# Kernel optimization log

Hardware: AMD Instinct MI355X
Metric: run time of the kernel (lower is better)

Reference implementation:

```python
import jax, jax.numpy as jnp
import numpy as np

T, B, D = 512, 64, 1024


def setup_inputs() -> dict:
    key = jax.random.key(0)
    k1, k2, k3, k4, k5 = jax.random.split(key, 5)
    s = 1.0 / np.sqrt(D)  # torch RNNCell init scale
    return {
        "x": jax.random.normal(k1, (T, B, D), dtype=jnp.float32),
        "W_ih": jax.random.normal(k2, (D, D), dtype=jnp.float32) * s,
        "W_hh": jax.random.normal(k3, (D, D), dtype=jnp.float32) * s,
        "b_ih": jax.random.normal(k4, (D,), dtype=jnp.float32) * s,
        "b_hh": jax.random.normal(k5, (D,), dtype=jnp.float32) * s,
    }


def reference(x, W_ih, W_hh, b_ih, b_hh):
    """CustomRNN forward: sequential Elman cell over time-major input.

    x: [T, B, D]; returns (output [T, B, D], final hidden [B, D]).
    """
    # Precompute the input projection for all timesteps in one big GEMM
    # (same math as per-step x_t @ W_ih^T + b_ih, just batched).
    xproj = jnp.einsum("tbd,hd->tbh", x, W_ih) + b_ih  # [T, B, D]

    def step(h, xp_t):
        h_new = jnp.tanh(xp_t + h @ W_hh.T + b_hh)  # [B, D]
        return h_new, h_new

    h0 = jnp.zeros((x.shape[1], W_hh.shape[0]), dtype=x.dtype)
    h_final, output = jax.lax.scan(step, h0, xproj)
    return output, h_final
```

## Files before the change

### kernel.cpp

```cpp
#include <hip/hip_runtime.h>
#include <hip/hip_bf16.h>

#define T_LEN 512
#define B_SZ  64
#define D_SZ  1024

typedef __attribute__((ext_vector_type(8))) short  short8;
typedef __attribute__((ext_vector_type(4))) float  f32x4;
typedef __attribute__((ext_vector_type(4))) unsigned short ushort4v;
typedef __attribute__((ext_vector_type(4))) unsigned int   uint4v;

__device__ __forceinline__ float bf2f(unsigned short u) {
    unsigned int x = ((unsigned int)u) << 16;
    return __uint_as_float(x);
}
__device__ __forceinline__ unsigned short f2bf(float f) {
    unsigned int x = __float_as_uint(f);
    unsigned int r = x + 0x7FFFu + ((x >> 16) & 1u);
    return (unsigned short)(r >> 16);
}
__device__ __forceinline__ void split2p(float f, unsigned short* hi, unsigned short* lo) {
    unsigned short h = f2bf(f);
    *hi = h;
    *lo = f2bf(f - bf2f(h));
}

#define CNT_STRIDE 64

__global__ void init_kernel(int* slot) {
    int i = threadIdx.x;
    if (i < 8 * CNT_STRIDE) slot[i] = 0;
}

#define BM 128
#define BN 128
#define BK 32
#define ASTR (BK + 8)

__global__ __launch_bounds__(256) void xproj_kernel(
    const float* __restrict__ x, const float* __restrict__ Wih,
    const float* __restrict__ bih, float* __restrict__ xp)
{
    __shared__ unsigned short Ah[BM][ASTR];
    __shared__ unsigned short Al[BM][ASTR];
    __shared__ unsigned short Bh[BN][ASTR];
    __shared__ unsigned short Bl[BN][ASTR];

    const int nblk = D_SZ / BN;
    const int bm = blockIdx.x / nblk;
    const int bn = blockIdx.x % nblk;
    const int m0 = bm * BM, n0 = bn * BN;
    const int tid  = threadIdx.x;
    const int lane = tid & 63, wave = tid >> 6;
    const int wm = wave >> 1, wn = wave & 1;

    f32x4 acc[4][4];
#pragma unroll
    for (int i = 0; i < 4; i++)
#pragma unroll
        for (int j = 0; j < 4; j++) acc[i][j] = (f32x4)0.0f;

    const int ar = lane & 15;
    const int kb = (lane >> 4) << 3;

    for (int k0 = 0; k0 < D_SZ; k0 += BK) {
#pragma unroll
        for (int i = 0; i < 4; i++) {
            int f4  = tid + i * 256;
            int row = f4 >> 3;
            int c4  = (f4 & 7) << 2;
            f32x4 va = *reinterpret_cast<const f32x4*>(x   + (size_t)(m0 + row) * D_SZ + k0 + c4);
            f32x4 vb = *reinterpret_cast<const f32x4*>(Wih + (size_t)(n0 + row) * D_SZ + k0 + c4);
            ushort4v pah, pal, pbh, pbl;
#pragma unroll
            for (int e = 0; e < 4; e++) {
                unsigned short h_, l_;
                split2p(va[e], &h_, &l_); pah[e] = h_; pal[e] = l_;
                split2p(vb[e], &h_, &l_); pbh[e] = h_; pbl[e] = l_;
            }
            *reinterpret_cast<ushort4v*>(&Ah[row][c4]) = pah;
            *reinterpret_cast<ushort4v*>(&Al[row][c4]) = pal;
            *reinterpret_cast<ushort4v*>(&Bh[row][c4]) = pbh;
            *reinterpret_cast<ushort4v*>(&Bl[row][c4]) = pbl;
        }
        __syncthreads();

        short8 ah[4], al[4], bh[4], bl[4];
#pragma unroll
        for (int mi = 0; mi < 4; mi++) {
            ah[mi] = *reinterpret_cast<const short8*>(&Ah[wm * 64 + mi * 16 + ar][kb]);
            al[mi] = *reinterpret_cast<const short8*>(&Al[wm * 64 + mi * 16 + ar][kb]);
        }
#pragma unroll
        for (int ni = 0; ni < 4; ni++) {
            bh[ni] = *reinterpret_cast<const short8*>(&Bh[wn * 64 + ni * 16 + ar][kb]);
            bl[ni] = *reinterpret_cast<const short8*>(&Bl[wn * 64 + ni * 16 + ar][kb]);
        }
#pragma unroll
        for (int mi = 0; mi < 4; mi++)
#pragma unroll
            for (int ni = 0; ni < 4; ni++) {
                acc[mi][ni] = __builtin_amdgcn_mfma_f32_16x16x32_bf16(ah[mi], bh[ni], acc[mi][ni], 0, 0, 0);
                acc[mi][ni] = __builtin_amdgcn_mfma_f32_16x16x32_bf16(al[mi], bh[ni], acc[mi][ni], 0, 0, 0);
                acc[mi][ni] = __builtin_amdgcn_mfma_f32_16x16x32_bf16(ah[mi], bl[ni], acc[mi][ni], 0, 0, 0);
            }
        __syncthreads();
    }

    const int r0 = (lane >> 4) * 4;
    const int cl = lane & 15;
#pragma unroll
    for (int mi = 0; mi < 4; mi++) {
#pragma unroll
        for (int ni = 0; ni < 4; ni++) {
            int col = n0 + wn * 64 + ni * 16 + cl;
            float bias = bih[col];
            size_t base = (size_t)(m0 + wm * 64 + mi * 16 + r0) * D_SZ + col;
#pragma unroll
            for (int r = 0; r < 4; r++)
                xp[base + (size_t)r * D_SZ] = acc[mi][ni][r] + bias;
        }
    }
}

#define MR 8
#define NC 32
#define HSTR (D_SZ + 8)

__global__ __launch_bounds__(128, 1) void rnn_kernel(
    const float* __restrict__ xp, const float* __restrict__ Whh,
    const float* __restrict__ bhh, float* __restrict__ out,
    unsigned int* hbuf, int* slot)
{
    __shared__ unsigned short Hh[16][HSTR];
    __shared__ unsigned short Hl[16][HSTR];
    __shared__ unsigned short Wlo[2][16][HSTR];

    const int wg = blockIdx.x;
    const int b  = wg & 7;
    const int c  = wg >> 3;
    const int tid  = threadIdx.x;
    const int lane = tid & 63, wave = tid >> 6;

    const int cl   = lane & 15;
    const int hi4  = lane >> 4;
    const int kb   = hi4 << 3;
    const int colg = c * NC + wave * 16 + cl;
    const float bias = bhh[colg];
    const int rloc = hi4 * 4;
    const bool active = (hi4 < 2);

    int* tslot = slot + b * CNT_STRIDE;

    short8 wh[32];
    {
        const float* wrow = Whh + (size_t)colg * D_SZ;
#pragma unroll
        for (int kk = 0; kk < 32; kk++) {
            f32x4 v0 = *reinterpret_cast<const f32x4*>(wrow + kk * 32 + kb);
            f32x4 v1 = *reinterpret_cast<const f32x4*>(wrow + kk * 32 + kb + 4);
            short8 sh, sl;
#pragma unroll
            for (int e = 0; e < 4; e++) {
                unsigned short h_, l_;
                split2p(v0[e], &h_, &l_); sh[e] = (short)h_; sl[e] = (short)l_;
                split2p(v1[e], &h_, &l_); sh[4 + e] = (short)h_; sl[4 + e] = (short)l_;
            }
            wh[kk] = sh;
            *reinterpret_cast<short8*>(&Wlo[wave][cl][kk * 32 + kb]) = sl;
        }
    }
    for (int i = tid; i < 16 * HSTR; i += 128) {
        (&Hh[0][0])[i] = 0;
        (&Hl[0][0])[i] = 0;
    }
    __syncthreads();

    for (int t = 0; t < T_LEN; t++) {
        float xv[4];
        const float* xpt = xp + ((size_t)t * B_SZ + b * MR) * D_SZ;
        if (active) {
#pragma unroll
            for (int r = 0; r < 4; r++)
                xv[r] = xpt[(size_t)(rloc + r) * D_SZ + colg];
        }

        if (t > 0) {
            if (wave == 0) {
                for (long it = 0; it < 200000000L; ++it) {
                    int v = __hip_atomic_load(tslot + (lane & 31), __ATOMIC_RELAXED, __HIP_MEMORY_SCOPE_AGENT);
                    if (__all(v >= t)) break;
                    __builtin_amdgcn_s_sleep(1);
                }
            }
            __syncthreads();
            const uint4v* hsrc16 = reinterpret_cast<const uint4v*>(
                hbuf + ((size_t)(t & 1) * B_SZ + b * MR) * D_SZ);
            uint4v vv[16];
#pragma unroll
            for (int i = 0; i < 16; i++) {
                asm volatile("global_load_dwordx4 %0, %1, off sc0 sc1"
                             : "=v"(vv[i]) : "v"(hsrc16 + tid + i * 128) : "memory");
            }
            asm volatile("s_waitcnt vmcnt(8)" ::: "memory");
            __builtin_amdgcn_sched_barrier(0);
#pragma unroll
            for (int i = 0; i < 8; i++) {
                int j   = tid + i * 128;
                int row = j >> 8;
                int c4  = (j & 255) << 2;
                ushort4v hh, hl;
#pragma unroll
                for (int e = 0; e < 4; e++) {
                    unsigned int u = vv[i][e];
                    hh[e] = (unsigned short)(u & 0xFFFFu);
                    hl[e] = (unsigned short)(u >> 16);
                }
                *reinterpret_cast<ushort4v*>(&Hh[row][c4]) = hh;
                *reinterpret_cast<ushort4v*>(&Hl[row][c4]) = hl;
            }
            asm volatile("s_waitcnt vmcnt(0)" ::: "memory");
            __builtin_amdgcn_sched_barrier(0);
#pragma unroll
            for (int i = 8; i < 16; i++) {
                int j   = tid + i * 128;
                int row = j >> 8;
                int c4  = (j & 255) << 2;
                ushort4v hh, hl;
#pragma unroll
                for (int e = 0; e < 4; e++) {
                    unsigned int u = vv[i][e];
                    hh[e] = (unsigned short)(u & 0xFFFFu);
                    hl[e] = (unsigned short)(u >> 16);
                }
                *reinterpret_cast<ushort4v*>(&Hh[row][c4]) = hh;
                *reinterpret_cast<ushort4v*>(&Hl[row][c4]) = hl;
            }
            __syncthreads();
        }

        f32x4 a0 = (f32x4)0.0f, a1 = (f32x4)0.0f, a2 = (f32x4)0.0f;
#pragma unroll
        for (int kk = 0; kk < 32; kk++) {
            short8 ah  = *reinterpret_cast<const short8*>(&Hh[cl][kk * 32 + kb]);
            short8 alo = *reinterpret_cast<const short8*>(&Hl[cl][kk * 32 + kb]);
            short8 wlv = *reinterpret_cast<const short8*>(&Wlo[wave][cl][kk * 32 + kb]);
            a0 = __builtin_amdgcn_mfma_f32_16x16x32_bf16(ah,  wh[kk], a0, 0, 0, 0);
            a1 = __builtin_amdgcn_mfma_f32_16x16x32_bf16(alo, wh[kk], a1, 0, 0, 0);
            a2 = __builtin_amdgcn_mfma_f32_16x16x32_bf16(ah,  wlv,    a2, 0, 0, 0);
        }

        float hval[4];
        if (active) {
            unsigned int* hdst = hbuf + ((size_t)((t + 1) & 1) * B_SZ + b * MR) * D_SZ;
#pragma unroll
            for (int r = 0; r < 4; r++) {
                int row = rloc + r;
                float pre = (a0[r] + a1[r] + a2[r]) + xv[r] + bias;
                float h = tanhf(pre);
                hval[r] = h;
                unsigned short hh_, ll_;
                split2p(h, &hh_, &ll_);
                unsigned int packed = (unsigned int)hh_ | ((unsigned int)ll_ << 16);
                __hip_atomic_store(&hdst[(size_t)row * D_SZ + colg], packed,
                                   __ATOMIC_RELAXED, __HIP_MEMORY_SCOPE_AGENT);
            }
        }
        asm volatile("s_waitcnt vmcnt(0)" ::: "memory");
        __syncthreads();
        if (tid == 0)
            __hip_atomic_store(tslot + c, t + 1, __ATOMIC_RELAXED, __HIP_MEMORY_SCOPE_AGENT);

        if (active) {
            float* outt = out + ((size_t)t * B_SZ + b * MR) * D_SZ;
#pragma unroll
            for (int r = 0; r < 4; r++) {
                int row = rloc + r;
                outt[(size_t)row * D_SZ + colg] = hval[r];
                if (t == T_LEN - 1)
                    out[(size_t)T_LEN * B_SZ * D_SZ + (size_t)(b * MR + row) * D_SZ + colg] = hval[r];
            }
        }
    }
}

extern "C" void kernel_launch(void* const* d_in, const int* in_sizes, int n_in,
                              void* d_out, int out_size, void* d_ws, size_t ws_size,
                              hipStream_t stream)
{
    const float* x   = (const float*)d_in[0];
    const float* Wih = (const float*)d_in[1];
    const float* Whh = (const float*)d_in[2];
    const float* bih = (const float*)d_in[3];
    const float* bhh = (const float*)d_in[4];
    float* out = (float*)d_out;

    char* ws = (char*)d_ws;
    float*        xp   = (float*)ws;
    unsigned int* hbuf = (unsigned int*)(ws + 134217728);
    int*          slot = (int*)(ws + 134217728 + 524288);

    init_kernel<<<dim3(1), dim3(512), 0, stream>>>(slot);
    xproj_kernel<<<dim3(2048), dim3(256), 0, stream>>>(x, Wih, bih, xp);
    rnn_kernel<<<dim3(256), dim3(128), 0, stream>>>(xp, Whh, bhh, out, hbuf, slot);
}
```

Measured before the change: 2.214 ms.

## Replace counter-slot barrier with per-element step tags embedded in hidden state

Removes the per-step flag-counter handshake, where each workgroup drained its stores, synchronized and published a counter that others polled. It instead embeds a 2-bit step tag in the low bits of the bf16 low-part of each packed hidden value and spins re-loading the hidden buffer until every tag matches. This cuts a full store-drain, barrier and atomic round-trip from the critical path of each timestep. The cost is slightly reduced precision in the low half, and repeated full-buffer reloads while waiting, which add memory traffic. There is also a bounded retry count that could silently proceed on stale data.

```diff
diff --git a/kernel.cpp b/kernel.cpp
--- a/kernel.cpp
+++ b/kernel.cpp
@@ -25,11 +25,10 @@
     *lo = f2bf(f - bf2f(h));
 }
 
-#define CNT_STRIDE 64
-
-__global__ void init_kernel(int* slot) {
-    int i = threadIdx.x;
-    if (i < 8 * CNT_STRIDE) slot[i] = 0;
+__global__ void init_kernel(uint4v* hb) {
+    int i = blockIdx.x * blockDim.x + threadIdx.x;
+    uint4v v; v[0] = v[1] = v[2] = v[3] = 0xFFFFFFFFu;
+    hb[i] = v;
 }
 
 #define BM 128
@@ -130,7 +129,7 @@
 __global__ __launch_bounds__(128, 1) void rnn_kernel(
     const float* __restrict__ xp, const float* __restrict__ Whh,
     const float* __restrict__ bhh, float* __restrict__ out,
-    unsigned int* hbuf, int* slot)
+    unsigned int* hbuf)
 {
     __shared__ unsigned short Hh[16][HSTR];
     __shared__ unsigned short Hl[16][HSTR];
@@ -150,8 +149,6 @@
     const int rloc = hi4 * 4;
     const bool active = (hi4 < 2);
 
-    int* tslot = slot + b * CNT_STRIDE;
-
     short8 wh[32];
     {
         const float* wrow = Whh + (size_t)colg * D_SZ;
@@ -186,26 +183,30 @@
         }
 
         if (t > 0) {
-            if (wave == 0) {
-                for (long it = 0; it < 200000000L; ++it) {
-                    int v = __hip_atomic_load(tslot + (lane & 31), __ATOMIC_RELAXED, __HIP_MEMORY_SCOPE_AGENT);
-                    if (__all(v >= t)) break;
-                    __builtin_amdgcn_s_sleep(1);
-                }
-            }
-            __syncthreads();
             const uint4v* hsrc16 = reinterpret_cast<const uint4v*>(
                 hbuf + ((size_t)(t & 1) * B_SZ + b * MR) * D_SZ);
+            const unsigned int want = (unsigned int)(t & 3);
             uint4v vv[16];
+            bool myok = false;
+            for (int tries = 0; tries < 20000; ++tries) {
+                if (!myok) {
+#pragma unroll
+                    for (int i = 0; i < 16; i++)
+                        asm volatile("global_load_dwordx4 %0, %1, off sc0 sc1"
+                                     : "=v"(vv[i]) : "v"(hsrc16 + tid + i * 128) : "memory");
+                    asm volatile("s_waitcnt vmcnt(0)" ::: "memory");
+                    unsigned int bad = 0;
+#pragma unroll
+                    for (int i = 0; i < 16; i++)
+#pragma unroll
+                        for (int e = 0; e < 4; e++)
+                            bad |= ((vv[i][e] >> 16) & 3u) ^ want;
+                    myok = (bad == 0);
+                }
+                if (__all(myok)) break;
+            }
 #pragma unroll
             for (int i = 0; i < 16; i++) {
-                asm volatile("global_load_dwordx4 %0, %1, off sc0 sc1"
-                             : "=v"(vv[i]) : "v"(hsrc16 + tid + i * 128) : "memory");
-            }
-            asm volatile("s_waitcnt vmcnt(8)" ::: "memory");
-            __builtin_amdgcn_sched_barrier(0);
-#pragma unroll
-            for (int i = 0; i < 8; i++) {
                 int j   = tid + i * 128;
                 int row = j >> 8;
                 int c4  = (j & 255) << 2;
@@ -214,24 +215,7 @@
                 for (int e = 0; e < 4; e++) {
                     unsigned int u = vv[i][e];
                     hh[e] = (unsigned short)(u & 0xFFFFu);
-                    hl[e] = (unsigned short)(u >> 16);
-                }
-                *reinterpret_cast<ushort4v*>(&Hh[row][c4]) = hh;
-                *reinterpret_cast<ushort4v*>(&Hl[row][c4]) = hl;
-            }
-            asm volatile("s_waitcnt vmcnt(0)" ::: "memory");
-            __builtin_amdgcn_sched_barrier(0);
-#pragma unroll
-            for (int i = 8; i < 16; i++) {
-                int j   = tid + i * 128;
-                int row = j >> 8;
-                int c4  = (j & 255) << 2;
-                ushort4v hh, hl;
-#pragma unroll
-                for (int e = 0; e < 4; e++) {
-                    unsigned int u = vv[i][e];
-                    hh[e] = (unsigned short)(u & 0xFFFFu);
-                    hl[e] = (unsigned short)(u >> 16);
+                    hl[e] = (unsigned short)((u >> 16) & 0xFFFCu);
                 }
                 *reinterpret_cast<ushort4v*>(&Hh[row][c4]) = hh;
                 *reinterpret_cast<ushort4v*>(&Hl[row][c4]) = hl;
@@ -253,6 +237,7 @@
         float hval[4];
         if (active) {
             unsigned int* hdst = hbuf + ((size_t)((t + 1) & 1) * B_SZ + b * MR) * D_SZ;
+            const unsigned int tag = (unsigned int)((t + 1) & 3) << 16;
 #pragma unroll
             for (int r = 0; r < 4; r++) {
                 int row = rloc + r;
@@ -261,15 +246,12 @@
                 hval[r] = h;
                 unsigned short hh_, ll_;
                 split2p(h, &hh_, &ll_);
-                unsigned int packed = (unsigned int)hh_ | ((unsigned int)ll_ << 16);
+                unsigned int packed = (unsigned int)hh_
+                                    | ((unsigned int)(ll_ & 0xFFFCu) << 16) | tag;
                 __hip_atomic_store(&hdst[(size_t)row * D_SZ + colg], packed,
                                    __ATOMIC_RELAXED, __HIP_MEMORY_SCOPE_AGENT);
             }
         }
-        asm volatile("s_waitcnt vmcnt(0)" ::: "memory");
-        __syncthreads();
-        if (tid == 0)
-            __hip_atomic_store(tslot + c, t + 1, __ATOMIC_RELAXED, __HIP_MEMORY_SCOPE_AGENT);
 
         if (active) {
             float* outt = out + ((size_t)t * B_SZ + b * MR) * D_SZ;
@@ -298,9 +280,8 @@
     char* ws = (char*)d_ws;
     float*        xp   = (float*)ws;
     unsigned int* hbuf = (unsigned int*)(ws + 134217728);
-    int*          slot = (int*)(ws + 134217728 + 524288);
-
-    init_kernel<<<dim3(1), dim3(512), 0, stream>>>(slot);
+
+    init_kernel<<<dim3(128), dim3(256), 0, stream>>>((uint4v*)hbuf);
     xproj_kernel<<<dim3(2048), dim3(256), 0, stream>>>(x, Wih, bih, xp);
-    rnn_kernel<<<dim3(256), dim3(128), 0, stream>>>(xp, Whh, bhh, out, hbuf, slot);
-}
+    rnn_kernel<<<dim3(256), dim3(128), 0, stream>>>(xp, Whh, bhh, out, hbuf);
+}
```

New measurement: 2.452 ms. 1.11x slower.

## Overlap second-half hidden-state load with first-half MFMAs, use fast tanh

Applied to the files above, without the earlier changes.

Reorders the per-step hidden-state global loads so the first half of the K dimension arrives first, then computes the first 16 k-steps of the recurrent MFMA while the second half is still in flight, with an extra barrier before the remaining k-steps. It also replaces tanhf with an exp/fast-divide tanh and moves the output stores into the same loop as the hidden publish. The goal is to hide global-load latency on the serial critical path and shorten the activation. In exchange there is one more barrier per step, slightly lower tanh accuracy, and the output stores now sit before the vmcnt wait that precedes the step-flag publish.

```diff
diff --git a/kernel.cpp b/kernel.cpp
--- a/kernel.cpp
+++ b/kernel.cpp
@@ -23,6 +23,11 @@
     unsigned short h = f2bf(f);
     *hi = h;
     *lo = f2bf(f - bf2f(h));
+}
+__device__ __forceinline__ float fast_tanh(float x) {
+    float xx = fminf(fmaxf(x, -20.0f), 20.0f);
+    float e2 = __expf(2.0f * xx);
+    return __fdividef(e2 - 1.0f, e2 + 1.0f);
 }
 
 #define CNT_STRIDE 64
@@ -185,6 +190,10 @@
                 xv[r] = xpt[(size_t)(rloc + r) * D_SZ + colg];
         }
 
+        uint4v vv[16];
+        const uint4v* hsrc16 = reinterpret_cast<const uint4v*>(
+            hbuf + ((size_t)(t & 1) * B_SZ + b * MR) * D_SZ);
+
         if (t > 0) {
             if (wave == 0) {
                 for (long it = 0; it < 200000000L; ++it) {
@@ -194,54 +203,33 @@
                 }
             }
             __syncthreads();
-            const uint4v* hsrc16 = reinterpret_cast<const uint4v*>(
-                hbuf + ((size_t)(t & 1) * B_SZ + b * MR) * D_SZ);
-            uint4v vv[16];
-#pragma unroll
-            for (int i = 0; i < 16; i++) {
+#pragma unroll
+            for (int s = 0; s < 16; s++) {
+                int i = (s < 8) ? (2 * s) : (2 * (s - 8) + 1);
                 asm volatile("global_load_dwordx4 %0, %1, off sc0 sc1"
-                             : "=v"(vv[i]) : "v"(hsrc16 + tid + i * 128) : "memory");
+                             : "=v"(vv[s]) : "v"(hsrc16 + tid + i * 128) : "memory");
             }
             asm volatile("s_waitcnt vmcnt(8)" ::: "memory");
             __builtin_amdgcn_sched_barrier(0);
 #pragma unroll
-            for (int i = 0; i < 8; i++) {
-                int j   = tid + i * 128;
-                int row = j >> 8;
-                int c4  = (j & 255) << 2;
+            for (int s = 0; s < 8; s++) {
+                int c4 = tid << 2;
                 ushort4v hh, hl;
 #pragma unroll
                 for (int e = 0; e < 4; e++) {
-                    unsigned int u = vv[i][e];
+                    unsigned int u = vv[s][e];
                     hh[e] = (unsigned short)(u & 0xFFFFu);
                     hl[e] = (unsigned short)(u >> 16);
                 }
-                *reinterpret_cast<ushort4v*>(&Hh[row][c4]) = hh;
-                *reinterpret_cast<ushort4v*>(&Hl[row][c4]) = hl;
-            }
-            asm volatile("s_waitcnt vmcnt(0)" ::: "memory");
-            __builtin_amdgcn_sched_barrier(0);
-#pragma unroll
-            for (int i = 8; i < 16; i++) {
-                int j   = tid + i * 128;
-                int row = j >> 8;
-                int c4  = (j & 255) << 2;
-                ushort4v hh, hl;
-#pragma unroll
-                for (int e = 0; e < 4; e++) {
-                    unsigned int u = vv[i][e];
-                    hh[e] = (unsigned short)(u & 0xFFFFu);
-                    hl[e] = (unsigned short)(u >> 16);
-                }
-                *reinterpret_cast<ushort4v*>(&Hh[row][c4]) = hh;
-                *reinterpret_cast<ushort4v*>(&Hl[row][c4]) = hl;
+                *reinterpret_cast<ushort4v*>(&Hh[s][c4]) = hh;
+                *reinterpret_cast<ushort4v*>(&Hl[s][c4]) = hl;
             }
             __syncthreads();
         }
 
         f32x4 a0 = (f32x4)0.0f, a1 = (f32x4)0.0f, a2 = (f32x4)0.0f;
 #pragma unroll
-        for (int kk = 0; kk < 32; kk++) {
+        for (int kk = 0; kk < 16; kk++) {
             short8 ah  = *reinterpret_cast<const short8*>(&Hh[cl][kk * 32 + kb]);
             short8 alo = *reinterpret_cast<const short8*>(&Hl[cl][kk * 32 + kb]);
             short8 wlv = *reinterpret_cast<const short8*>(&Wlo[wave][cl][kk * 32 + kb]);
@@ -250,37 +238,57 @@
             a2 = __builtin_amdgcn_mfma_f32_16x16x32_bf16(ah,  wlv,    a2, 0, 0, 0);
         }
 
-        float hval[4];
+        if (t > 0) {
+            asm volatile("s_waitcnt vmcnt(0)" ::: "memory");
+            __builtin_amdgcn_sched_barrier(0);
+#pragma unroll
+            for (int s = 0; s < 8; s++) {
+                int c4 = 512 + (tid << 2);
+                ushort4v hh, hl;
+#pragma unroll
+                for (int e = 0; e < 4; e++) {
+                    unsigned int u = vv[s + 8][e];
+                    hh[e] = (unsigned short)(u & 0xFFFFu);
+                    hl[e] = (unsigned short)(u >> 16);
+                }
+                *reinterpret_cast<ushort4v*>(&Hh[s][c4]) = hh;
+                *reinterpret_cast<ushort4v*>(&Hl[s][c4]) = hl;
+            }
+            __syncthreads();
+        }
+
+#pragma unroll
+        for (int kk = 16; kk < 32; kk++) {
+            short8 ah  = *reinterpret_cast<const short8*>(&Hh[cl][kk * 32 + kb]);
+            short8 alo = *reinterpret_cast<const short8*>(&Hl[cl][kk * 32 + kb]);
+            short8 wlv = *reinterpret_cast<const short8*>(&Wlo[wave][cl][kk * 32 + kb]);
+            a0 = __builtin_amdgcn_mfma_f32_16x16x32_bf16(ah,  wh[kk], a0, 0, 0, 0);
+            a1 = __builtin_amdgcn_mfma_f32_16x16x32_bf16(alo, wh[kk], a1, 0, 0, 0);
+            a2 = __builtin_amdgcn_mfma_f32_16x16x32_bf16(ah,  wlv,    a2, 0, 0, 0);
+        }
+
         if (active) {
             unsigned int* hdst = hbuf + ((size_t)((t + 1) & 1) * B_SZ + b * MR) * D_SZ;
+            float* outt = out + ((size_t)t * B_SZ + b * MR) * D_SZ;
 #pragma unroll
             for (int r = 0; r < 4; r++) {
                 int row = rloc + r;
                 float pre = (a0[r] + a1[r] + a2[r]) + xv[r] + bias;
-                float h = tanhf(pre);
-                hval[r] = h;
+                float h = fast_tanh(pre);
                 unsigned short hh_, ll_;
                 split2p(h, &hh_, &ll_);
                 unsigned int packed = (unsigned int)hh_ | ((unsigned int)ll_ << 16);
                 __hip_atomic_store(&hdst[(size_t)row * D_SZ + colg], packed,
                                    __ATOMIC_RELAXED, __HIP_MEMORY_SCOPE_AGENT);
+                outt[(size_t)row * D_SZ + colg] = h;
+                if (t == T_LEN - 1)
+                    out[(size_t)T_LEN * B_SZ * D_SZ + (size_t)(b * MR + row) * D_SZ + colg] = h;
             }
         }
         asm volatile("s_waitcnt vmcnt(0)" ::: "memory");
         __syncthreads();
         if (tid == 0)
             __hip_atomic_store(tslot + c, t + 1, __ATOMIC_RELAXED, __HIP_MEMORY_SCOPE_AGENT);
-
-        if (active) {
-            float* outt = out + ((size_t)t * B_SZ + b * MR) * D_SZ;
-#pragma unroll
-            for (int r = 0; r < 4; r++) {
-                int row = rloc + r;
-                outt[(size_t)row * D_SZ + colg] = hval[r];
-                if (t == T_LEN - 1)
-                    out[(size_t)T_LEN * B_SZ * D_SZ + (size_t)(b * MR + row) * D_SZ + colg] = hval[r];
-            }
-        }
     }
 }
 
```

Result: no change. 2.243 ms (+1.3%).
